# Kernel tuning notes

Hardware: AMD Instinct MI355X
Metric: run time of the kernel (lower is better)

Reference implementation:

```python
import jax, jax.numpy as jnp
import numpy as np

HIDDEN = 4096
NUM_HEADS = 32
HEAD_DIM = HIDDEN // NUM_HEADS  # 128, used only as softmax scale
CACHE_LEN = 100
BATCH = 8192


def setup_inputs() -> dict:
    key = jax.random.key(0)
    ks = jax.random.split(key, 7)
    return {
        "x": jax.random.normal(ks[0], (BATCH, HIDDEN), dtype=jnp.float32),
        "q_w": jax.random.normal(ks[1], (HIDDEN, HIDDEN), dtype=jnp.float32) * (1.0 / np.sqrt(HIDDEN)),
        "q_b": jax.random.normal(ks[2], (HIDDEN,), dtype=jnp.float32) * 0.01,
        "k_cache": jax.random.normal(ks[3], (CACHE_LEN, HIDDEN), dtype=jnp.float32),
        "v_cache": jax.random.normal(ks[4], (CACHE_LEN, HIDDEN), dtype=jnp.float32),
        "out_w": jax.random.normal(ks[5], (HIDDEN, HIDDEN), dtype=jnp.float32) * (1.0 / np.sqrt(HIDDEN)),
        "out_b": jax.random.normal(ks[6], (HIDDEN,), dtype=jnp.float32) * 0.01,
    }


def reference(x, q_w, q_b, k_cache, v_cache, out_w, out_b):
    # q_proj: torch Linear -> x @ W^T + b
    q = x @ q_w.T + q_b                                   # [N, H]
    # concat one zero row onto each cache (kv_len = CACHE_LEN + 1)
    k = jnp.concatenate([k_cache, jnp.zeros_like(k_cache[:1])], axis=0)  # [L+1, H]
    v = jnp.concatenate([v_cache, jnp.zeros_like(v_cache[:1])], axis=0)  # [L+1, H]
    scale = 1.0 / np.sqrt(HEAD_DIM).astype(np.float32)
    scores = (q @ k.T) * scale                            # [N, L+1]
    weights = jax.nn.softmax(scores, axis=-1)
    attn = weights @ v                                    # [N, H]
    return attn @ out_w.T + out_b                         # [N, H]
```

## Files before the change

kernel.cpp:

```cpp
#include <hip/hip_runtime.h>
#include <cstdio>

typedef __attribute__((ext_vector_type(8))) short short8;
typedef __attribute__((ext_vector_type(4))) float f32x4;


__device__ __forceinline__ unsigned short bf16r(float f) {
  union { float f; unsigned int u; } x; x.f = f;
  unsigned int r = x.u + 0x7fffu + ((x.u >> 16) & 1u);
  return (unsigned short)(r >> 16);
}

__device__ __forceinline__ float bf16f(unsigned short h) {
  union { unsigned int u; float f; } x; x.u = ((unsigned int)h) << 16;
  return x.f;
}

__device__ __forceinline__ void gload_lds16(const void* g, void* l) {
  __builtin_amdgcn_global_load_lds((const __attribute__((address_space(1))) void*)g,
                                   (__attribute__((address_space(3))) void*)l,
                                   16, 0, 0);
}

__device__ __forceinline__ short8 pack_bf16(float4 f0, float4 f1) {
  short8 h;
  h[0] = (short)bf16r(f0.x); h[1] = (short)bf16r(f0.y);
  h[2] = (short)bf16r(f0.z); h[3] = (short)bf16r(f0.w);
  h[4] = (short)bf16r(f1.x); h[5] = (short)bf16r(f1.y);
  h[6] = (short)bf16r(f1.z); h[7] = (short)bf16r(f1.w);
  return h;
}


__global__ void prep(const float* __restrict__ kc, const float* __restrict__ vc,
                     const float* __restrict__ qb,
                     unsigned short* __restrict__ kpad, unsigned short* __restrict__ vpad,
                     float* __restrict__ sbias) {
  const int b = blockIdx.x, tid = threadIdx.x;
  if (b < 4096) {
    const bool isK = b < 2048;
    const int bb = isK ? b : b - 2048;
    int idx = bb * 256 + tid;
    int row = idx >> 12;
    const float* src = isK ? kc : vc;
    float v = (row < 100) ? src[idx] : 0.f;
    (isK ? kpad : vpad)[idx] = bf16r(v);
  } else {
    const int wave = tid >> 6, lane = tid & 63;
    const int l = (b - 4096) * 4 + wave;
    float s = 0.f;
    if (l < 100) {
      for (int i = lane * 4; i < 4096; i += 256) {
        float4 k = *reinterpret_cast<const float4*>(kc + (size_t)l * 4096 + i);
        float4 q = *reinterpret_cast<const float4*>(qb + i);
        s += k.x * q.x + k.y * q.y + k.z * q.z + k.w * q.w;
      }
    }
    #pragma unroll
    for (int off = 1; off < 64; off <<= 1) s += __shfl_xor(s, off);
    if (lane == 0) sbias[l] = s;
  }
}


__device__ __forceinline__ void kq_fused_body(const unsigned short* __restrict__ Kp,
                                              const float* __restrict__ Qw,
                                              float* __restrict__ Cpart,
                                              int H, int jchunk, int js, int itile,
                                              char* smem) {
  unsigned short (*Ak)[32] = (unsigned short (*)[32])smem;
  float (*Ts)[129] = (float (*)[129])(smem + 8192);

  const int tid = threadIdx.x, wave = tid >> 6, lane = tid & 63;
  const int wm = wave >> 1, wn = wave & 1;
  const int j0 = js * jchunk;
  const int i0 = itile * 128;

  const int sr = wave * 16 + (lane >> 2);
  const int sc = (lane & 3) << 3;
  const unsigned short* Kp0 = Kp + (size_t)sr * H + j0 + sc;
  const unsigned short* Kp1 = Kp + (size_t)(64 + sr) * H + j0 + sc;
  unsigned short* AD0 = &Ak[wave * 16][0];
  unsigned short* AD1 = &Ak[64 + wave * 16][0];

  const int tj = tid >> 3;
  const int tc = (tid & 7) * 16;
  const float* Qp = Qw + (size_t)(j0 + tj) * H + i0 + tc;

  const int fr = lane & 15;
  const int kq = lane >> 4;

  f32x4 acc[4][4] = {};

  for (int jj = 0; jj < jchunk; jj += 32) {
    gload_lds16(Kp0 + jj, AD0);
    gload_lds16(Kp1 + jj, AD1);
    {
      const float* q = Qp + (size_t)jj * H;
      float4 v0 = *reinterpret_cast<const float4*>(q);
      float4 v1 = *reinterpret_cast<const float4*>(q + 4);
      float4 v2 = *reinterpret_cast<const float4*>(q + 8);
      float4 v3 = *reinterpret_cast<const float4*>(q + 12);
      Ts[tj][tc + 0]  = v0.x; Ts[tj][tc + 1]  = v0.y; Ts[tj][tc + 2]  = v0.z; Ts[tj][tc + 3]  = v0.w;
      Ts[tj][tc + 4]  = v1.x; Ts[tj][tc + 5]  = v1.y; Ts[tj][tc + 6]  = v1.z; Ts[tj][tc + 7]  = v1.w;
      Ts[tj][tc + 8]  = v2.x; Ts[tj][tc + 9]  = v2.y; Ts[tj][tc + 10] = v2.z; Ts[tj][tc + 11] = v2.w;
      Ts[tj][tc + 12] = v3.x; Ts[tj][tc + 13] = v3.y; Ts[tj][tc + 14] = v3.z; Ts[tj][tc + 15] = v3.w;
    }
    __syncthreads();

    short8 av[4];
    #pragma unroll
    for (int mi = 0; mi < 4; ++mi)
      av[mi] = *reinterpret_cast<const short8*>(&Ak[wm * 64 + mi * 16 + fr][kq * 8]);

    short8 bhi[4], blo[4];
    #pragma unroll
    for (int ni = 0; ni < 4; ++ni) {
      const int ic = wn * 64 + ni * 16 + fr;
      #pragma unroll
      for (int s = 0; s < 8; ++s) {
        float f = Ts[kq * 8 + s][ic];
        unsigned short h = bf16r(f);
        bhi[ni][s] = (short)h;
        blo[ni][s] = (short)bf16r(f - bf16f(h));
      }
    }

    #pragma unroll
    for (int mi = 0; mi < 4; ++mi)
      #pragma unroll
      for (int ni = 0; ni < 4; ++ni) {
        acc[mi][ni] = __builtin_amdgcn_mfma_f32_16x16x32_bf16(av[mi], bhi[ni], acc[mi][ni], 0, 0, 0);
        acc[mi][ni] = __builtin_amdgcn_mfma_f32_16x16x32_bf16(av[mi], blo[ni], acc[mi][ni], 0, 0, 0);
      }
    __syncthreads();
  }

  float* Cp = Cpart + (size_t)js * 128 * H;
  const int orow = (lane >> 4) * 4;
  const int ocol = lane & 15;
  #pragma unroll
  for (int mi = 0; mi < 4; ++mi) {
    #pragma unroll
    for (int ni = 0; ni < 4; ++ni) {
      size_t r0 = (size_t)wm * 64 + mi * 16 + orow;
      size_t c  = (size_t)i0 + wn * 64 + ni * 16 + ocol;
      #pragma unroll
      for (int j = 0; j < 4; ++j)
        Cp[(r0 + j) * (size_t)H + c] = acc[mi][ni][j];
    }
  }
}


template<int NB, int MT>
__device__ __forceinline__ void gemm_sv_body(const float* __restrict__ A,
                                             const unsigned short* __restrict__ B,
                                             float* __restrict__ Cpart,
                                             int M, int Kstride, int kchunk,
                                             int ks, int mblk, char* smem) {
  constexpr int FOLD = NB / 128;
  constexpr int MFRAG = MT / 32;
  static_assert(MT / 32 + NB / 64 == 6, "vmcnt count must be 6");
  float (*As)[MT][32] = (float (*)[MT][32])smem;
  unsigned short (*Bs)[NB][32] = (unsigned short (*)[NB][32])(smem + 2 * MT * 32 * 4);

  const int tid = threadIdx.x, wave = tid >> 6, lane = tid & 63;
  const int wm = wave >> 1, wn = wave & 1;
  const size_t rowA0 = (size_t)mblk * MT;
  const int k0 = ks * kchunk;
  const int nsteps = kchunk >> 5;

  const int ar = lane >> 3;
  const int as_g = (lane & 7) ^ ar;
  const int br = lane >> 2;
  const int bs_g = (lane & 3) ^ (br & 3);

#define STAGE_SV(kt, BUF) do { \
    const int _kc = k0 + (kt) * 32; \
    _Pragma("unroll") \
    for (int j = 0; j < MT / 32; ++j) \
      gload_lds16(A + (rowA0 + wave * (MT / 4) + j * 8 + ar) * (size_t)Kstride + _kc + as_g * 4, \
                  &As[BUF][wave * (MT / 4) + j * 8][0]); \
    _Pragma("unroll") \
    for (int j = 0; j < NB / 64; ++j) \
      gload_lds16(B + (size_t)(wave * (NB / 4) + j * 16 + br) * Kstride + _kc + bs_g * 8, \
                  &Bs[BUF][wave * (NB / 4) + j * 16][0]); \
  } while (0)

#define WAIT_STAGE asm volatile("s_waitcnt vmcnt(6)" ::: "memory")

  const int fr = lane & 15, kq = lane >> 4;
  f32x4 acc[MFRAG][4] = {};

  STAGE_SV(0, 0);
  STAGE_SV(1, 1);
  WAIT_STAGE;
  asm volatile("" ::: "memory");
  __builtin_amdgcn_s_barrier();
  asm volatile("" ::: "memory");

  for (int k = 0; k < nsteps; ++k) {
    const int c = k & 1;

    short8 av[MFRAG], bv[4][FOLD];
    #pragma unroll
    for (int mi = 0; mi < MFRAG; ++mi) {
      const float* rp = &As[c][wm * (MT / 2) + mi * 16 + fr][0];
      float4 f0 = *reinterpret_cast<const float4*>(rp + (((2 * kq)     ^ (fr & 7)) * 4));
      float4 f1 = *reinterpret_cast<const float4*>(rp + (((2 * kq + 1) ^ (fr & 7)) * 4));
      av[mi] = pack_bf16(f0, f1);
    }
    #pragma unroll
    for (int ni = 0; ni < 4; ++ni)
      #pragma unroll
      for (int p = 0; p < FOLD; ++p) {
        int rb = p * 128 + wn * 64 + ni * 16 + fr;
        bv[ni][p] = *reinterpret_cast<const short8*>(&Bs[c][rb][0] + ((kq ^ (fr & 3)) * 8));
      }

    asm volatile("s_waitcnt lgkmcnt(0)" ::: "memory");
    __builtin_amdgcn_s_barrier();
    asm volatile("" ::: "memory");

    const int kt2 = (k + 2 < nsteps) ? k + 2 : nsteps - 1;
    STAGE_SV(kt2, c);
    asm volatile("" ::: "memory");

    __builtin_amdgcn_s_setprio(1);
    #pragma unroll
    for (int mi = 0; mi < MFRAG; ++mi)
      #pragma unroll
      for (int ni = 0; ni < 4; ++ni)
        #pragma unroll
        for (int p = 0; p < FOLD; ++p)
          acc[mi][ni] = __builtin_amdgcn_mfma_f32_16x16x32_bf16(av[mi], bv[ni][p], acc[mi][ni], 0, 0, 0);
    __builtin_amdgcn_s_setprio(0);

    WAIT_STAGE;
    asm volatile("" ::: "memory");
    __builtin_amdgcn_s_barrier();
    asm volatile("" ::: "memory");
  }

#undef STAGE_SV
#undef WAIT_STAGE

  float* Cp = Cpart + (size_t)ks * M * 128;
  const int orow = (lane >> 4) * 4;
  const int ocol = lane & 15;
  #pragma unroll
  for (int mi = 0; mi < MFRAG; ++mi) {
    #pragma unroll
    for (int ni = 0; ni < 4; ++ni) {
      size_t r0 = rowA0 + wm * (MT / 2) + mi * 16 + orow;
      size_t c  = (size_t)wn * 64 + ni * 16 + ocol;
      #pragma unroll
      for (int j = 0; j < 4; ++j)
        Cp[(r0 + j) * 128 + c] = acc[mi][ni][j];
    }
  }
}


__global__ __launch_bounds__(256, 1)
void fused_kqvo(const unsigned short* __restrict__ kpad, const float* __restrict__ qw,
                float* __restrict__ KQpart,
                const float* __restrict__ outw, const unsigned short* __restrict__ vpad,
                float* __restrict__ VOpart, int H) {
  __shared__ __align__(16) char smem[49152];
  const int b = blockIdx.x;
  if (b < 256) {
    kq_fused_body(kpad, qw, KQpart, H, 512, b & 7, b >> 3, smem);
  } else {
    const int b2 = b - 256;
    gemm_sv_body<128, 128>(outw, vpad, VOpart, H, H, 512, b2 & 7, b2 >> 3, smem);
  }
}


__global__ __launch_bounds__(256, 1)
void gemm_s(const float* __restrict__ A, const unsigned short* __restrict__ B,
            float* __restrict__ Cpart, int M, int Kstride, int kchunk) {
  __shared__ __align__(16) char smem[49152];
  gemm_sv_body<256, 64>(A, B, Cpart, M, Kstride, kchunk, blockIdx.x, blockIdx.y, smem);
}


__global__ void reduces(const float* __restrict__ KQpart, unsigned short* __restrict__ KQ2,
                        const float* __restrict__ VOpart, unsigned short* __restrict__ VOT2) {
  const int b = blockIdx.x;
  if (b < 2048) {
    int idx = b * 256 + threadIdx.x;
    float s = 0.f;
    #pragma unroll
    for (int ks = 0; ks < 8; ++ks) s += KQpart[(size_t)ks * 128 * 4096 + idx];
    unsigned short hi = bf16r(s);
    unsigned short lo = bf16r(s - bf16f(hi));
    int l = idx >> 12, j = idx & 4095;
    KQ2[(size_t)l * 4096 + j]         = hi;
    KQ2[(size_t)(l + 128) * 4096 + j] = lo;
  } else {
    int idx = (b - 2048) * 256 + threadIdx.x;
    float s = 0.f;
    #pragma unroll
    for (int ks = 0; ks < 8; ++ks) s += VOpart[(size_t)ks * 4096 * 128 + idx];
    unsigned short hi = bf16r(s);
    unsigned short lo = bf16r(s - bf16f(hi));
    int o = idx >> 7, l = idx & 127;
    VOT2[(size_t)o * 256 + l]       = hi;
    VOT2[(size_t)o * 256 + 128 + l] = lo;
  }
}


__global__ void softmax_fused2(const float* __restrict__ Spart, const float* __restrict__ sbias,
                               unsigned short* __restrict__ W2, int rows) {
  int wave = threadIdx.x >> 6;
  int lane = threadIdx.x & 63;
  int row = blockIdx.x * (blockDim.x >> 6) + wave;
  if (row >= rows) return;
  const float scale = 0.088388347648318447f;
  float sx = 0.f, sy = 0.f;
  #pragma unroll
  for (int ks = 0; ks < 4; ++ks) {
    float2 p = reinterpret_cast<const float2*>(Spart + ((size_t)ks * rows + row) * 128)[lane];
    sx += p.x; sy += p.y;
  }
  float2 bb = reinterpret_cast<const float2*>(sbias)[lane];
  sx += bb.x; sy += bb.y;
  int c0 = lane * 2, c1 = c0 + 1;
  float s0 = (c0 <= 100) ? sx * scale : -1e30f;
  float s1 = (c1 <= 100) ? sy * scale : -1e30f;
  float m = fmaxf(s0, s1);
  #pragma unroll
  for (int off = 1; off < 64; off <<= 1) m = fmaxf(m, __shfl_xor(m, off));
  float e0 = (c0 <= 100) ? __expf(s0 - m) : 0.f;
  float e1 = (c1 <= 100) ? __expf(s1 - m) : 0.f;
  float sum = e0 + e1;
  #pragma unroll
  for (int off = 1; off < 64; off <<= 1) sum += __shfl_xor(sum, off);
  float inv = 1.f / sum;
  ushort2 o;
  o.x = bf16r(e0 * inv);
  o.y = bf16r(e1 * inv);
  reinterpret_cast<ushort2*>(W2 + (size_t)row * 256)[lane] = o;
  reinterpret_cast<ushort2*>(W2 + (size_t)row * 256 + 128)[lane] = o;
}


__global__ __launch_bounds__(256)
void gemm_final(const unsigned short* __restrict__ A,
                const unsigned short* __restrict__ B,
                const float* __restrict__ bias,
                float* __restrict__ Cout,
                int M, int N, int K) {
  __shared__ unsigned short As[128][40];
  __shared__ unsigned short Bs[128][40];

  const int tid = threadIdx.x, wave = tid >> 6, lane = tid & 63;
  const int wm = wave >> 1, wn = wave & 1;
  const size_t rowA0 = (size_t)blockIdx.y * 128;
  const size_t colB0 = (size_t)blockIdx.x * 128;

  f32x4 acc[4][4] = {};

  const int srow  = tid >> 1;
  const int shalf = (tid & 1) * 16;

  const unsigned short* Ap = A + (rowA0 + srow) * (size_t)K + shalf;
  const unsigned short* Bp = B + (colB0 + srow) * (size_t)K + shalf;

  const int fr = lane & 15;
  const int fk = (lane >> 4) << 3;

  for (int k0 = 0; k0 < K; k0 += 32) {
    short8 a0 = *reinterpret_cast<const short8*>(Ap + k0);
    short8 a1 = *reinterpret_cast<const short8*>(Ap + k0 + 8);
    short8 b0 = *reinterpret_cast<const short8*>(Bp + k0);
    short8 b1 = *reinterpret_cast<const short8*>(Bp + k0 + 8);
    *reinterpret_cast<short8*>(&As[srow][shalf])     = a0;
    *reinterpret_cast<short8*>(&As[srow][shalf + 8]) = a1;
    *reinterpret_cast<short8*>(&Bs[srow][shalf])     = b0;
    *reinterpret_cast<short8*>(&Bs[srow][shalf + 8]) = b1;
    __syncthreads();

    short8 av[4], bv[4];
    #pragma unroll
    for (int mi = 0; mi < 4; ++mi)
      av[mi] = *reinterpret_cast<const short8*>(&As[wm * 64 + mi * 16 + fr][fk]);
    #pragma unroll
    for (int ni = 0; ni < 4; ++ni)
      bv[ni] = *reinterpret_cast<const short8*>(&Bs[wn * 64 + ni * 16 + fr][fk]);
    #pragma unroll
    for (int mi = 0; mi < 4; ++mi)
      #pragma unroll
      for (int ni = 0; ni < 4; ++ni)
        acc[mi][ni] = __builtin_amdgcn_mfma_f32_16x16x32_bf16(av[mi], bv[ni], acc[mi][ni], 0, 0, 0);
    __syncthreads();
  }

  const int orow = (lane >> 4) * 4;
  const int ocol = lane & 15;
  #pragma unroll
  for (int mi = 0; mi < 4; ++mi) {
    #pragma unroll
    for (int ni = 0; ni < 4; ++ni) {
      size_t r0 = rowA0 + wm * 64 + mi * 16 + orow;
      size_t c  = colB0 + wn * 64 + ni * 16 + ocol;
      float bv_ = bias[c];
      #pragma unroll
      for (int j = 0; j < 4; ++j)
        Cout[(r0 + j) * (size_t)N + c] = acc[mi][ni][j] + bv_;
    }
  }
}


extern "C" void kernel_launch(void* const* d_in, const int* in_sizes, int n_in,
                              void* d_out, int out_size, void* d_ws, size_t ws_size,
                              hipStream_t stream) {
  const float* x       = (const float*)d_in[0];
  const float* q_w     = (const float*)d_in[1];
  const float* q_b     = (const float*)d_in[2];
  const float* k_cache = (const float*)d_in[3];
  const float* v_cache = (const float*)d_in[4];
  const float* out_w   = (const float*)d_in[5];
  const float* out_b   = (const float*)d_in[6];
  float* out = (float*)d_out;

  const int M = 8192, H = 4096;

  char* ws = (char*)d_ws;
  size_t off = 0;
  auto alloc = [&](size_t bytes) { void* p = ws + off; off += (bytes + 255) & ~(size_t)255; return p; };
  unsigned short* kpad   = (unsigned short*)alloc((size_t)128 * H * 2);
  unsigned short* vpad   = (unsigned short*)alloc((size_t)128 * H * 2);
  float*          sbias  = (float*)alloc(128 * 4);
  unsigned short* KQ2    = (unsigned short*)alloc((size_t)256 * H * 2);
  unsigned short* W2     = (unsigned short*)alloc((size_t)M * 256 * 2);
  unsigned short* VOT2   = (unsigned short*)alloc((size_t)H * 256 * 2);
  float*          KQpart = (float*)alloc((size_t)8 * 128 * H * 4);
  float*          VOpart = (float*)alloc((size_t)8 * H * 128 * 4);
  float*          Spart  = VOpart;
  if (ws_size < off) { fprintf(stderr, "ws too small: need %zu have %zu\n", off, ws_size); return; }

  prep<<<4128, 256, 0, stream>>>(k_cache, v_cache, q_b, kpad, vpad, sbias);

  fused_kqvo<<<512, 256, 0, stream>>>(kpad, q_w, KQpart, out_w, vpad, VOpart, H);

  reduces<<<4096, 256, 0, stream>>>(KQpart, KQ2, VOpart, VOT2);

  gemm_s<<<dim3(4, 128), 256, 0, stream>>>(x, KQ2, Spart, M, H, 1024);

  softmax_fused2<<<M / 4, 256, 0, stream>>>(Spart, sbias, W2, M);

  gemm_final<<<dim3(32, 64), 256, 0, stream>>>(W2, VOT2, out_b, out, M, H, 256);
}
```

Measured before the change: 162.2 us.

## Double-buffer KQ loads and deepen GEMM pipeline to three LDS stages

New measurement: 169.3 us. 1.04x slower.

```diff
diff --git a/kernel.cpp b/kernel.cpp
--- a/kernel.cpp
+++ b/kernel.cpp
@@ -68,20 +68,19 @@
                                               float* __restrict__ Cpart,
                                               int H, int jchunk, int js, int itile,
                                               char* smem) {
-  unsigned short (*Ak)[32] = (unsigned short (*)[32])smem;
-  float (*Ts)[129] = (float (*)[129])(smem + 8192);
+  unsigned short (*Ak)[128][32] = (unsigned short (*)[128][32])smem;
+  float (*Ts)[32][129] = (float (*)[32][129])(smem + 16384);
 
   const int tid = threadIdx.x, wave = tid >> 6, lane = tid & 63;
   const int wm = wave >> 1, wn = wave & 1;
   const int j0 = js * jchunk;
   const int i0 = itile * 128;
+  const int nsteps = jchunk >> 5;
 
   const int sr = wave * 16 + (lane >> 2);
   const int sc = (lane & 3) << 3;
   const unsigned short* Kp0 = Kp + (size_t)sr * H + j0 + sc;
   const unsigned short* Kp1 = Kp + (size_t)(64 + sr) * H + j0 + sc;
-  unsigned short* AD0 = &Ak[wave * 16][0];
-  unsigned short* AD1 = &Ak[64 + wave * 16][0];
 
   const int tj = tid >> 3;
   const int tc = (tid & 7) * 16;
@@ -90,51 +89,93 @@
   const int fr = lane & 15;
   const int kq = lane >> 4;
 
+  float4 qa0, qa1, qa2, qa3;
+  float4 qb0, qb1, qb2, qb3;
+
+#define KSTAGE(step, buf) do { \
+    gload_lds16(Kp0 + (step) * 32, &Ak[buf][wave * 16][0]); \
+    gload_lds16(Kp1 + (step) * 32, &Ak[buf][64 + wave * 16][0]); \
+  } while (0)
+
+#define QLOAD(r0, r1, r2, r3, step) do { \
+    const float* _q = Qp + (size_t)(step) * 32 * H; \
+    r0 = *reinterpret_cast<const float4*>(_q); \
+    r1 = *reinterpret_cast<const float4*>(_q + 4); \
+    r2 = *reinterpret_cast<const float4*>(_q + 8); \
+    r3 = *reinterpret_cast<const float4*>(_q + 12); \
+  } while (0)
+
+#define TSWRITE(buf, r0, r1, r2, r3) do { \
+    float* _t = &Ts[buf][tj][tc]; \
+    _t[0]  = r0.x; _t[1]  = r0.y; _t[2]  = r0.z; _t[3]  = r0.w; \
+    _t[4]  = r1.x; _t[5]  = r1.y; _t[6]  = r1.z; _t[7]  = r1.w; \
+    _t[8]  = r2.x; _t[9]  = r2.y; _t[10] = r2.z; _t[11] = r2.w; \
+    _t[12] = r3.x; _t[13] = r3.y; _t[14] = r3.z; _t[15] = r3.w; \
+  } while (0)
+
+#define KQ_PHASE(C, N, QW0, QW1, QW2, QW3, QL0, QL1, QL2, QL3, k) do { \
+    short8 av[4]; \
+    _Pragma("unroll") \
+    for (int mi = 0; mi < 4; ++mi) \
+      av[mi] = *reinterpret_cast<const short8*>(&Ak[C][wm * 64 + mi * 16 + fr][kq * 8]); \
+    short8 bhi[4], blo[4]; \
+    _Pragma("unroll") \
+    for (int ni = 0; ni < 4; ++ni) { \
+      const int ic = wn * 64 + ni * 16 + fr; \
+      _Pragma("unroll") \
+      for (int s = 0; s < 8; ++s) { \
+        float f = Ts[C][kq * 8 + s][ic]; \
+        unsigned short h = bf16r(f); \
+        bhi[ni][s] = (short)h; \
+        blo[ni][s] = (short)bf16r(f - bf16f(h)); \
+      } \
+    } \
+    asm volatile("s_waitcnt lgkmcnt(0)" ::: "memory"); \
+    __builtin_amdgcn_s_barrier(); \
+    asm volatile("" ::: "memory"); \
+    { const int _s2 = ((k) + 2 < nsteps) ? (k) + 2 : nsteps - 1; \
+      KSTAGE(_s2, C); } \
+    asm volatile("s_waitcnt vmcnt(2)" ::: "memory"); \
+    asm volatile("" ::: "memory"); \
+    TSWRITE(N, QW0, QW1, QW2, QW3); \
+    { const int _s2 = ((k) + 2 < nsteps) ? (k) + 2 : nsteps - 1; \
+      QLOAD(QL0, QL1, QL2, QL3, _s2); } \
+    __builtin_amdgcn_s_setprio(1); \
+    _Pragma("unroll") \
+    for (int mi = 0; mi < 4; ++mi) \
+      _Pragma("unroll") \
+      for (int ni = 0; ni < 4; ++ni) { \
+        acc[mi][ni] = __builtin_amdgcn_mfma_f32_16x16x32_bf16(av[mi], bhi[ni], acc[mi][ni], 0, 0, 0); \
+        acc[mi][ni] = __builtin_amdgcn_mfma_f32_16x16x32_bf16(av[mi], blo[ni], acc[mi][ni], 0, 0, 0); \
+      } \
+    __builtin_amdgcn_s_setprio(0); \
+    asm volatile("s_waitcnt lgkmcnt(0)" ::: "memory"); \
+    __builtin_amdgcn_s_barrier(); \
+    asm volatile("" ::: "memory"); \
+  } while (0)
+
   f32x4 acc[4][4] = {};
 
-  for (int jj = 0; jj < jchunk; jj += 32) {
-    gload_lds16(Kp0 + jj, AD0);
-    gload_lds16(Kp1 + jj, AD1);
-    {
-      const float* q = Qp + (size_t)jj * H;
-      float4 v0 = *reinterpret_cast<const float4*>(q);
-      float4 v1 = *reinterpret_cast<const float4*>(q + 4);
-      float4 v2 = *reinterpret_cast<const float4*>(q + 8);
-      float4 v3 = *reinterpret_cast<const float4*>(q + 12);
-      Ts[tj][tc + 0]  = v0.x; Ts[tj][tc + 1]  = v0.y; Ts[tj][tc + 2]  = v0.z; Ts[tj][tc + 3]  = v0.w;
-      Ts[tj][tc + 4]  = v1.x; Ts[tj][tc + 5]  = v1.y; Ts[tj][tc + 6]  = v1.z; Ts[tj][tc + 7]  = v1.w;
-      Ts[tj][tc + 8]  = v2.x; Ts[tj][tc + 9]  = v2.y; Ts[tj][tc + 10] = v2.z; Ts[tj][tc + 11] = v2.w;
-      Ts[tj][tc + 12] = v3.x; Ts[tj][tc + 13] = v3.y; Ts[tj][tc + 14] = v3.z; Ts[tj][tc + 15] = v3.w;
-    }
-    __syncthreads();
-
-    short8 av[4];
-    #pragma unroll
-    for (int mi = 0; mi < 4; ++mi)
-      av[mi] = *reinterpret_cast<const short8*>(&Ak[wm * 64 + mi * 16 + fr][kq * 8]);
-
-    short8 bhi[4], blo[4];
-    #pragma unroll
-    for (int ni = 0; ni < 4; ++ni) {
-      const int ic = wn * 64 + ni * 16 + fr;
-      #pragma unroll
-      for (int s = 0; s < 8; ++s) {
-        float f = Ts[kq * 8 + s][ic];
-        unsigned short h = bf16r(f);
-        bhi[ni][s] = (short)h;
-        blo[ni][s] = (short)bf16r(f - bf16f(h));
-      }
-    }
-
-    #pragma unroll
-    for (int mi = 0; mi < 4; ++mi)
-      #pragma unroll
-      for (int ni = 0; ni < 4; ++ni) {
-        acc[mi][ni] = __builtin_amdgcn_mfma_f32_16x16x32_bf16(av[mi], bhi[ni], acc[mi][ni], 0, 0, 0);
-        acc[mi][ni] = __builtin_amdgcn_mfma_f32_16x16x32_bf16(av[mi], blo[ni], acc[mi][ni], 0, 0, 0);
-      }
-    __syncthreads();
-  }
+  QLOAD(qa0, qa1, qa2, qa3, 0);
+  KSTAGE(0, 0);
+  QLOAD(qb0, qb1, qb2, qb3, 1);
+  KSTAGE(1, 1);
+  asm volatile("s_waitcnt vmcnt(6)" ::: "memory");
+  asm volatile("" ::: "memory");
+  TSWRITE(0, qa0, qa1, qa2, qa3);
+  asm volatile("s_waitcnt lgkmcnt(0)" ::: "memory");
+  __builtin_amdgcn_s_barrier();
+  asm volatile("" ::: "memory");
+
+  for (int k = 0; k < nsteps; k += 2) {
+    KQ_PHASE(0, 1, qb0, qb1, qb2, qb3, qa0, qa1, qa2, qa3, k);
+    KQ_PHASE(1, 0, qa0, qa1, qa2, qa3, qb0, qb1, qb2, qb3, k + 1);
+  }
+
+#undef KSTAGE
+#undef QLOAD
+#undef TSWRITE
+#undef KQ_PHASE
 
   float* Cp = Cpart + (size_t)js * 128 * H;
   const int orow = (lane >> 4) * 4;
@@ -161,9 +202,9 @@
                                              int ks, int mblk, char* smem) {
   constexpr int FOLD = NB / 128;
   constexpr int MFRAG = MT / 32;
-  static_assert(MT / 32 + NB / 64 == 6, "vmcnt count must be 6");
+  static_assert(MT / 32 + NB / 64 == 6, "stage ops per thread must be 6");
   float (*As)[MT][32] = (float (*)[MT][32])smem;
-  unsigned short (*Bs)[NB][32] = (unsigned short (*)[NB][32])(smem + 2 * MT * 32 * 4);
+  unsigned short (*Bs)[NB][32] = (unsigned short (*)[NB][32])(smem + 3 * MT * 32 * 4);
 
   const int tid = threadIdx.x, wave = tid >> 6, lane = tid & 63;
   const int wm = wave >> 1, wn = wave & 1;
@@ -188,21 +229,21 @@
                   &Bs[BUF][wave * (NB / 4) + j * 16][0]); \
   } while (0)
 
-#define WAIT_STAGE asm volatile("s_waitcnt vmcnt(6)" ::: "memory")
+#define WAIT_STAGE asm volatile("s_waitcnt vmcnt(12)" ::: "memory")
 
   const int fr = lane & 15, kq = lane >> 4;
   f32x4 acc[MFRAG][4] = {};
 
   STAGE_SV(0, 0);
   STAGE_SV(1, 1);
+  STAGE_SV(2, 2);
   WAIT_STAGE;
   asm volatile("" ::: "memory");
   __builtin_amdgcn_s_barrier();
   asm volatile("" ::: "memory");
 
+  int c = 0;
   for (int k = 0; k < nsteps; ++k) {
-    const int c = k & 1;
-
     short8 av[MFRAG], bv[4][FOLD];
     #pragma unroll
     for (int mi = 0; mi < MFRAG; ++mi) {
@@ -223,8 +264,8 @@
     __builtin_amdgcn_s_barrier();
     asm volatile("" ::: "memory");
 
-    const int kt2 = (k + 2 < nsteps) ? k + 2 : nsteps - 1;
-    STAGE_SV(kt2, c);
+    const int kt3 = (k + 3 < nsteps) ? k + 3 : nsteps - 1;
+    STAGE_SV(kt3, c);
     asm volatile("" ::: "memory");
 
     __builtin_amdgcn_s_setprio(1);
@@ -241,6 +282,8 @@
     asm volatile("" ::: "memory");
     __builtin_amdgcn_s_barrier();
     asm volatile("" ::: "memory");
+
+    c = (c == 2) ? 0 : c + 1;
   }
 
 #undef STAGE_SV
@@ -254,10 +297,10 @@
     #pragma unroll
     for (int ni = 0; ni < 4; ++ni) {
       size_t r0 = rowA0 + wm * (MT / 2) + mi * 16 + orow;
-      size_t c  = (size_t)wn * 64 + ni * 16 + ocol;
+      size_t c2 = (size_t)wn * 64 + ni * 16 + ocol;
       #pragma unroll
       for (int j = 0; j < 4; ++j)
-        Cp[(r0 + j) * 128 + c] = acc[mi][ni][j];
+        Cp[(r0 + j) * 128 + c2] = acc[mi][ni][j];
     }
   }
 }
@@ -268,7 +311,7 @@
                 float* __restrict__ KQpart,
                 const float* __restrict__ outw, const unsigned short* __restrict__ vpad,
                 float* __restrict__ VOpart, int H) {
-  __shared__ __align__(16) char smem[49152];
+  __shared__ __align__(16) char smem[73728];
   const int b = blockIdx.x;
   if (b < 256) {
     kq_fused_body(kpad, qw, KQpart, H, 512, b & 7, b >> 3, smem);
@@ -282,7 +325,7 @@
 __global__ __launch_bounds__(256, 1)
 void gemm_s(const float* __restrict__ A, const unsigned short* __restrict__ B,
             float* __restrict__ Cpart, int M, int Kstride, int kchunk) {
-  __shared__ __align__(16) char smem[49152];
+  __shared__ __align__(16) char smem[73728];
   gemm_sv_body<256, 64>(A, B, Cpart, M, Kstride, kchunk, blockIdx.x, blockIdx.y, smem);
 }
 
```
